# Kernel tuning notes

Hardware: AMD Instinct MI355X
Metric: run time of the kernel (lower is better)

Reference implementation:

```python
import jax, jax.numpy as jnp
import numpy as np

T = 19          # TIME_STEPS from the source
N = 20000
EMB = 64        # embedding_dim
HID = 128       # hidden_dim
SCALE = 4.0     # InputEmbedding scale
ENC_STEPS = 8   # LRP code: encoder weights for t < 8, decoder after


def setup_inputs():
    key = jax.random.key(0)
    ks = jax.random.split(key, 16)
    obs = jax.random.normal(ks[0], (T, N, 2), dtype=jnp.float32) * 5.0
    # tracks appear at random start times -> NaN before start (drives track_mask)
    starts = jax.random.randint(ks[1], (N,), 0, 10)
    active = jnp.arange(T)[:, None] >= starts[None, :]
    obs = jnp.where(active[:, :, None], obs, jnp.nan)
    goals = jax.random.normal(ks[2], (N, 2), dtype=jnp.float32)

    def p(k, shape):
        return jax.random.normal(k, shape, dtype=jnp.float32) * 0.05

    return {
        "obs": obs, "goals": goals,
        "w_emb": p(ks[3], (EMB, 2)), "b_emb": p(ks[4], (EMB,)),
        "w_ih_e": p(ks[5], (4 * HID, EMB)), "b_ih_e": p(ks[6], (4 * HID,)),
        "w_hh_e": p(ks[7], (4 * HID, HID)), "b_hh_e": p(ks[8], (4 * HID,)),
        "w_ih_d": p(ks[9], (4 * HID, EMB)), "b_ih_d": p(ks[10], (4 * HID,)),
        "w_hh_d": p(ks[11], (4 * HID, HID)), "b_hh_d": p(ks[12], (4 * HID,)),
        "w_out": p(ks[13], (5, HID)), "b_out": p(ks[14], (5,)),
    }


def _lstm_cell(x, h, c, w_ih, b_ih, w_hh, b_hh):
    # torch.nn.LSTMCell: gate order i, f, g, o
    gates = x @ w_ih.T + b_ih + h @ w_hh.T + b_hh  # [n, 4H]
    i, f, g, o = jnp.split(gates, 4, axis=-1)
    i, f, o = jax.nn.sigmoid(i), jax.nn.sigmoid(f), jax.nn.sigmoid(o)
    g = jnp.tanh(g)
    c2 = f * c + i * g
    h2 = o * jnp.tanh(c2)
    return h2, c2


def _hidden2normal(h, w_out, b_out):
    n = h @ w_out.T + b_out  # [n, 5]
    return jnp.concatenate([
        n[:, :2],
        0.01 + 0.2 * jax.nn.sigmoid(n[:, 2:4]),  # sigmas
        0.7 * jax.nn.sigmoid(n[:, 4:5]),          # rho
    ], axis=1)


def _run_steps(obs1_seq, obs2_seq, h, c, w_emb, b_emb, w_ih, b_ih, w_hh, b_hh, w_out, b_out):
    def step(carry, ob):
        h, c = carry
        o1, o2 = ob
        # track_mask: active iff neither position is NaN (masked gather in torch)
        mask = ~(jnp.isnan(o1[:, 0]) | jnp.isnan(o2[:, 0]))
        m = mask[:, None]
        vel = jnp.where(m, o2 - o1, 0.0)                      # sanitize NaNs
        emb = jax.nn.relu((vel * SCALE) @ w_emb.T + b_emb)    # InputEmbedding
        h2, c2 = _lstm_cell(emb, h, c, w_ih, b_ih, w_hh, b_hh)
        normal = jnp.where(m, _hidden2normal(h2, w_out, b_out), 0.0)
        # scatter updated state back only for active tracks
        return (jnp.where(m, h2, h), jnp.where(m, c2, c)), normal

    (h, c), normals = jax.lax.scan(step, (h, c), (obs1_seq, obs2_seq))
    return h, c, normals


def reference(obs, goals, w_emb, b_emb, w_ih_e, b_ih_e, w_hh_e, b_hh_e,
              w_ih_d, b_ih_d, w_hh_d, b_hh_d, w_out, b_out):
    del goals  # goal_flag=False: goal embedding branch disabled
    n = obs.shape[1]
    h = jnp.zeros((n, HID), dtype=obs.dtype)
    c = jnp.zeros((n, HID), dtype=obs.dtype)
    o1, o2 = obs[:-1], obs[1:]
    h, c, n_enc = _run_steps(o1[:ENC_STEPS], o2[:ENC_STEPS], h, c,
                             w_emb, b_emb, w_ih_e, b_ih_e, w_hh_e, b_hh_e, w_out, b_out)
    h, c, n_dec = _run_steps(o1[ENC_STEPS:], o2[ENC_STEPS:], h, c,
                             w_emb, b_emb, w_ih_d, b_ih_d, w_hh_d, b_hh_d, w_out, b_out)
    return jnp.concatenate([n_enc, n_dec], axis=0)  # [T-1, N, 5]
```

## Files before the change

kernel.cpp:

```cpp
#include <hip/hip_runtime.h>

#define T_OUT 18
#define NAG   20000
#define EMBD  64
#define HIDD  128
#define APB   80
#define MT    5
#define SH    136
#define SE    72

typedef _Float16 half8 __attribute__((ext_vector_type(8)));
typedef float    f32x4 __attribute__((ext_vector_type(4)));

__device__ __forceinline__ float rcpf(float x) { return __builtin_amdgcn_rcpf(x); }
__device__ __forceinline__ float sigmf(float x) { return rcpf(1.0f + __expf(-x)); }

__global__ __launch_bounds__(512, 2)
void lstm_seq_kernel(
    const float* __restrict__ obs,
    const float* __restrict__ w_emb,  const float* __restrict__ b_emb,
    const float* __restrict__ w_ih_e, const float* __restrict__ b_ih_e,
    const float* __restrict__ w_hh_e, const float* __restrict__ b_hh_e,
    const float* __restrict__ w_ih_d, const float* __restrict__ b_ih_d,
    const float* __restrict__ w_hh_d, const float* __restrict__ b_hh_d,
    const float* __restrict__ w_out,  const float* __restrict__ b_out,
    float* __restrict__ out)
{
  __shared__ __align__(16) _Float16 h_s[2][APB * SH];
  __shared__ __align__(16) _Float16 e_s[2][APB * SE];
  __shared__ float mask_s[3][APB];

  const int tid = threadIdx.x;
  const int wv  = tid >> 6;
  const int ln  = tid & 63;
  const int l15 = ln & 15;
  const int lg  = ln >> 4;
  const int a0  = blockIdx.x * APB;
  const float2* obs2 = (const float2*)obs;

  for (int i = tid; i < APB * SH; i += 512) h_s[0][i] = (_Float16)0.f;

  const float we0 = 4.f * w_emb[ln * 2 + 0];
  const float we1 = 4.f * w_emb[ln * 2 + 1];
  const float be  = b_emb[ln];

  half8 fih[4][2];
  half8 fhh[4][4];
  half8 fout[4];
  float bsum[4], bo;

  {
    int j = l15;
    #pragma unroll
    for (int ks = 0; ks < 4; ks++) {
      half8 v;
      #pragma unroll
      for (int q = 0; q < 8; q++) {
        float x = (j < 5) ? w_out[j * HIDD + ks * 32 + lg * 8 + q] : 0.f;
        v[q] = (_Float16)x;
      }
      fout[ks] = v;
    }
    bo = (j < 5) ? b_out[j] : 0.f;
  }

  auto load_phase = [&](const float* wih, const float* bih,
                        const float* whh, const float* bhh) {
    #pragma unroll
    for (int n = 0; n < 4; n++) {
      int row = n * 128 + wv * 16 + l15;
      #pragma unroll
      for (int ks = 0; ks < 2; ks++) {
        const float* p = wih + row * EMBD + ks * 32 + lg * 8;
        half8 v;
        #pragma unroll
        for (int q = 0; q < 8; q++) v[q] = (_Float16)p[q];
        fih[n][ks] = v;
      }
      #pragma unroll
      for (int ks = 0; ks < 4; ks++) {
        const float* p = whh + row * HIDD + ks * 32 + lg * 8;
        half8 v;
        #pragma unroll
        for (int q = 0; q < 8; q++) v[q] = (_Float16)p[q];
        fhh[n][ks] = v;
      }
      bsum[n] = bih[row] + bhh[row];
    }
  };

  auto emb_mask = [&](int buf, int ts) {
    float vx_ = 0.f, vy_ = 0.f, ok_ = 0.f;
    if (ln < 10) {
      int a = a0 + wv + 8 * ln;
      float2 o1 = obs2[(size_t)ts * NAG + a];
      float2 o2 = obs2[(size_t)(ts + 1) * NAG + a];
      bool ok = !__builtin_isnan(o1.x) && !__builtin_isnan(o2.x);
      vx_ = ok ? (o2.x - o1.x) : 0.f;
      vy_ = ok ? (o2.y - o1.y) : 0.f;
      ok_ = ok ? 1.f : 0.f;
      mask_s[ts % 3][wv + 8 * ln] = ok_;
    }
    #pragma unroll
    for (int k = 0; k < 10; k++) {
      float vx = __shfl(vx_, k, 64);
      float vy = __shfl(vy_, k, 64);
      int a = wv + 8 * k;
      float e = fmaf(vx, we0, fmaf(vy, we1, be));
      e_s[buf][a * SE + ln] = (_Float16)fmaxf(e, 0.f);
    }
  };

  load_phase(w_ih_e, b_ih_e, w_hh_e, b_hh_e);
  emb_mask(0, 0);
  __syncthreads();

  float c_r[MT][4];
  float h_r[MT][4];
  #pragma unroll
  for (int m = 0; m < MT; m++)
    #pragma unroll
    for (int r = 0; r < 4; r++) { c_r[m][r] = 0.f; h_r[m][r] = 0.f; }

  const int hid = wv * 16 + l15;

  #pragma unroll 1
  for (int t = 0; t < T_OUT; t++) {
    if (t == 8) load_phase(w_ih_d, b_ih_d, w_hh_d, b_hh_d);

    const int idx  = t & 1;
    const int nidx = idx ^ 1;
    const int msC  = t % 3;
    const int msP  = (t + 2) % 3;

    #pragma unroll
    for (int m = 0; m < MT; m++) {
      f32x4 acc[4];
      #pragma unroll
      for (int n = 0; n < 4; n++)
        acc[n] = f32x4{bsum[n], bsum[n], bsum[n], bsum[n]};

      #pragma unroll
      for (int ks = 0; ks < 2; ks++) {
        half8 av = *(const half8*)&e_s[idx][(m * 16 + l15) * SE + ks * 32 + lg * 8];
        #pragma unroll
        for (int n = 0; n < 4; n++)
          acc[n] = __builtin_amdgcn_mfma_f32_16x16x32_f16(av, fih[n][ks], acc[n], 0, 0, 0);
      }
      #pragma unroll
      for (int ks = 0; ks < 4; ks++) {
        half8 av = *(const half8*)&h_s[idx][(m * 16 + l15) * SH + ks * 32 + lg * 8];
        #pragma unroll
        for (int n = 0; n < 4; n++)
          acc[n] = __builtin_amdgcn_mfma_f32_16x16x32_f16(av, fhh[n][ks], acc[n], 0, 0, 0);
      }

      float c2a[4], ova[4];
      #pragma unroll
      for (int r = 0; r < 4; r++) {
        float ai = acc[0][r], af = acc[1][r];
        float ag_ = acc[2][r], ao = acc[3][r];
        float ei = __expf(-ai), ef = __expf(-af);
        float eo = __expf(-ao), eg = __expf(-2.f * ag_);
        float di = 1.f + ei, df = 1.f + ef, dd = 1.f + eo, dg = 1.f + eg;
        float p1 = rcpf(di * df);
        float iv = df * p1, fv = di * p1;
        float p2 = rcpf(dd * dg);
        float ov = dg * p2;
        float gv = fmaf(2.f, dd * p2, -1.f);
        c2a[r] = fmaf(fv, c_r[m][r], iv * gv);
        ova[r] = ov;
      }
      float dc[4];
      #pragma unroll
      for (int r = 0; r < 4; r++) dc[r] = 1.f + __expf(-2.f * c2a[r]);
      float q01 = rcpf(dc[0] * dc[1]);
      float q23 = rcpf(dc[2] * dc[3]);
      float inv[4] = { dc[1] * q01, dc[0] * q01, dc[3] * q23, dc[2] * q23 };
      #pragma unroll
      for (int r = 0; r < 4; r++) {
        int ag = m * 16 + lg * 4 + r;
        float mk = mask_s[msC][ag];
        float th = fmaf(2.f, inv[r], -1.f);
        float h2 = ova[r] * th;
        bool on = (mk != 0.f);
        c_r[m][r] = on ? c2a[r] : c_r[m][r];
        _Float16 hh = (_Float16)(on ? h2 : h_r[m][r]);
        h_s[nidx][ag * SH + hid] = hh;
        h_r[m][r] = (float)hh;
      }
    }

    if (t > 0 && wv < 5) {
      f32x4 oa = f32x4{bo, bo, bo, bo};
      #pragma unroll
      for (int ks = 0; ks < 4; ks++) {
        half8 av = *(const half8*)&h_s[idx][(wv * 16 + l15) * SH + ks * 32 + lg * 8];
        oa = __builtin_amdgcn_mfma_f32_16x16x32_f16(av, fout[ks], oa, 0, 0, 0);
      }
      int j = l15;
      #pragma unroll
      for (int r = 0; r < 4; r++) {
        int ag = wv * 16 + lg * 4 + r;
        float mk = mask_s[msP][ag];
        float nv = oa[r];
        float y;
        if (j < 2)      y = nv;
        else if (j < 4) y = 0.01f + 0.2f * sigmf(nv);
        else            y = 0.7f * sigmf(nv);
        if (j < 5) out[((size_t)(t - 1) * NAG + a0 + ag) * 5 + j] = y * mk;
      }
    }

    if (t + 1 < T_OUT) emb_mask(nidx, t + 1);

    __syncthreads();
  }

  if (wv < 5) {
    f32x4 oa = f32x4{bo, bo, bo, bo};
    #pragma unroll
    for (int ks = 0; ks < 4; ks++) {
      half8 av = *(const half8*)&h_s[T_OUT & 1][(wv * 16 + l15) * SH + ks * 32 + lg * 8];
      oa = __builtin_amdgcn_mfma_f32_16x16x32_f16(av, fout[ks], oa, 0, 0, 0);
    }
    int j = l15;
    #pragma unroll
    for (int r = 0; r < 4; r++) {
      int ag = wv * 16 + lg * 4 + r;
      float mk = mask_s[(T_OUT - 1) % 3][ag];
      float nv = oa[r];
      float y;
      if (j < 2)      y = nv;
      else if (j < 4) y = 0.01f + 0.2f * sigmf(nv);
      else            y = 0.7f * sigmf(nv);
      if (j < 5) out[((size_t)(T_OUT - 1) * NAG + a0 + ag) * 5 + j] = y * mk;
    }
  }
}

extern "C" void kernel_launch(void* const* d_in, const int* in_sizes, int n_in,
                              void* d_out, int out_size, void* d_ws, size_t ws_size,
                              hipStream_t stream) {
  const float* obs    = (const float*)d_in[0];
  const float* w_emb  = (const float*)d_in[2];
  const float* b_emb  = (const float*)d_in[3];
  const float* w_ih_e = (const float*)d_in[4];
  const float* b_ih_e = (const float*)d_in[5];
  const float* w_hh_e = (const float*)d_in[6];
  const float* b_hh_e = (const float*)d_in[7];
  const float* w_ih_d = (const float*)d_in[8];
  const float* b_ih_d = (const float*)d_in[9];
  const float* w_hh_d = (const float*)d_in[10];
  const float* b_hh_d = (const float*)d_in[11];
  const float* w_out  = (const float*)d_in[12];
  const float* b_out  = (const float*)d_in[13];
  float* out = (float*)d_out;

  lstm_seq_kernel<<<dim3(250), dim3(512), 0, stream>>>(
      obs, w_emb, b_emb, w_ih_e, b_ih_e, w_hh_e, b_hh_e,
      w_ih_d, b_ih_d, w_hh_d, b_hh_d, w_out, b_out, out);
}
```

Measured before the change: 139.3 us.

## Prefetch observations two steps ahead with dedicated owner threads and shared velocity buffer

New measurement: 134.6 us. 3.4% less time.

```diff
diff --git a/kernel.cpp b/kernel.cpp
--- a/kernel.cpp
+++ b/kernel.cpp
@@ -5,7 +5,6 @@
 #define EMBD  64
 #define HIDD  128
 #define APB   80
-#define MT    5
 #define SH    136
 #define SE    72
 
@@ -28,7 +27,8 @@
 {
   __shared__ __align__(16) _Float16 h_s[2][APB * SH];
   __shared__ __align__(16) _Float16 e_s[2][APB * SE];
-  __shared__ float mask_s[3][APB];
+  __shared__ float vel_s[2][APB * 2];
+  __shared__ float mask_s[4][APB];
 
   const int tid = threadIdx.x;
   const int wv  = tid >> 6;
@@ -36,6 +36,8 @@
   const int l15 = ln & 15;
   const int lg  = ln >> 4;
   const int a0  = blockIdx.x * APB;
+  const int po  = tid - 320;
+  const bool obsOwner = ((unsigned)po) < APB;
   const float2* obs2 = (const float2*)obs;
 
   for (int i = tid; i < APB * SH; i += 512) h_s[0][i] = (_Float16)0.f;
@@ -43,6 +45,23 @@
   const float we0 = 4.f * w_emb[ln * 2 + 0];
   const float we1 = 4.f * w_emb[ln * 2 + 1];
   const float be  = b_emb[ln];
+
+  float oAx = 0.f, oAy = 0.f;
+  if (obsOwner) {
+    int a = a0 + po;
+    float2 o0 = obs2[0 * NAG + a];
+    float2 o1 = obs2[1 * NAG + a];
+    float2 o2 = obs2[2 * NAG + a];
+    bool k0 = !__builtin_isnan(o0.x) && !__builtin_isnan(o1.x);
+    bool k1 = !__builtin_isnan(o1.x) && !__builtin_isnan(o2.x);
+    mask_s[0][po] = k0 ? 1.f : 0.f;
+    vel_s[0][po * 2 + 0] = k0 ? (o1.x - o0.x) : 0.f;
+    vel_s[0][po * 2 + 1] = k0 ? (o1.y - o0.y) : 0.f;
+    mask_s[1][po] = k1 ? 1.f : 0.f;
+    vel_s[1][po * 2 + 0] = k1 ? (o2.x - o1.x) : 0.f;
+    vel_s[1][po * 2 + 1] = k1 ? (o2.y - o1.y) : 0.f;
+    oAx = o2.x; oAy = o2.y;
+  }
 
   half8 fih[4][2];
   half8 fhh[4][4];
@@ -89,36 +108,25 @@
     }
   };
 
-  auto emb_mask = [&](int buf, int ts) {
-    float vx_ = 0.f, vy_ = 0.f, ok_ = 0.f;
-    if (ln < 10) {
-      int a = a0 + wv + 8 * ln;
-      float2 o1 = obs2[(size_t)ts * NAG + a];
-      float2 o2 = obs2[(size_t)(ts + 1) * NAG + a];
-      bool ok = !__builtin_isnan(o1.x) && !__builtin_isnan(o2.x);
-      vx_ = ok ? (o2.x - o1.x) : 0.f;
-      vy_ = ok ? (o2.y - o1.y) : 0.f;
-      ok_ = ok ? 1.f : 0.f;
-      mask_s[ts % 3][wv + 8 * ln] = ok_;
-    }
+  auto emb_compute = [&](int ebuf, int vbuf) {
     #pragma unroll
     for (int k = 0; k < 10; k++) {
-      float vx = __shfl(vx_, k, 64);
-      float vy = __shfl(vy_, k, 64);
       int a = wv + 8 * k;
+      float vx = vel_s[vbuf][a * 2], vy = vel_s[vbuf][a * 2 + 1];
       float e = fmaf(vx, we0, fmaf(vy, we1, be));
-      e_s[buf][a * SE + ln] = (_Float16)fmaxf(e, 0.f);
+      e_s[ebuf][a * SE + ln] = (_Float16)fmaxf(e, 0.f);
     }
   };
 
   load_phase(w_ih_e, b_ih_e, w_hh_e, b_hh_e);
-  emb_mask(0, 0);
   __syncthreads();
-
-  float c_r[MT][4];
-  float h_r[MT][4];
+  emb_compute(0, 0);
+  __syncthreads();
+
+  float c_r[5][4];
+  float h_r[5][4];
   #pragma unroll
-  for (int m = 0; m < MT; m++)
+  for (int m = 0; m < 5; m++)
     #pragma unroll
     for (int r = 0; r < 4; r++) { c_r[m][r] = 0.f; h_r[m][r] = 0.f; }
 
@@ -130,11 +138,17 @@
 
     const int idx  = t & 1;
     const int nidx = idx ^ 1;
-    const int msC  = t % 3;
-    const int msP  = (t + 2) % 3;
-
-    #pragma unroll
-    for (int m = 0; m < MT; m++) {
+    const int msC  = t & 3;
+    const int msP  = (t + 3) & 3;
+
+    float n3x = 0.f, n3y = 0.f;
+    if (t + 2 < T_OUT && obsOwner) {
+      float2 o = obs2[(size_t)(t + 3) * NAG + a0 + po];
+      n3x = o.x; n3y = o.y;
+    }
+
+    #pragma unroll
+    for (int m = 0; m < 5; m++) {
       f32x4 acc[4];
       #pragma unroll
       for (int n = 0; n < 4; n++)
@@ -212,7 +226,15 @@
       }
     }
 
-    if (t + 1 < T_OUT) emb_mask(nidx, t + 1);
+    if (t + 1 < T_OUT) emb_compute(nidx, (t + 1) & 1);
+
+    if (t + 2 < T_OUT && obsOwner) {
+      bool ok = !__builtin_isnan(oAx) && !__builtin_isnan(n3x);
+      mask_s[(t + 2) & 3][po] = ok ? 1.f : 0.f;
+      vel_s[t & 1][po * 2 + 0] = ok ? (n3x - oAx) : 0.f;
+      vel_s[t & 1][po * 2 + 1] = ok ? (n3y - oAy) : 0.f;
+      oAx = n3x; oAy = n3y;
+    }
 
     __syncthreads();
   }
@@ -228,7 +250,7 @@
     #pragma unroll
     for (int r = 0; r < 4; r++) {
       int ag = wv * 16 + lg * 4 + r;
-      float mk = mask_s[(T_OUT - 1) % 3][ag];
+      float mk = mask_s[(T_OUT - 1) & 3][ag];
       float nv = oa[r];
       float y;
       if (j < 2)      y = nv;
```
